# Optimization experiments

Hardware: AMD Instinct MI355X
Metric: run time of the kernel (lower is better)

## Reference

```python
import jax, jax.numpy as jnp
import numpy as np

WS = 4          # window size per axis
HEADS = 3
HEAD_DIM = 32
DIM = 96
DISP = WS // 2  # displacement for shifted windows


def _make_mask(axis):
    # (w^3, w^3) additive mask, -inf across the wrap-around boundary on `axis`
    m = np.zeros((WS, WS, WS, WS, WS, WS), dtype=np.float32)
    d = DISP
    if axis == 0:
        m[-d:, :, :, :-d, :, :] = -np.inf
        m[:-d, :, :, -d:, :, :] = -np.inf
    elif axis == 1:
        m[:, -d:, :, :, :-d, :] = -np.inf
        m[:, :-d, :, :, -d:, :] = -np.inf
    else:
        m[:, :, -d:, :, :, :-d] = -np.inf
        m[:, :, :-d, :, :, -d:] = -np.inf
    return jnp.asarray(m.reshape(WS**3, WS**3))


def setup_inputs() -> dict:
    key = jax.random.key(0)
    k1, k2, k3, k4 = jax.random.split(key, 4)
    inner = HEADS * HEAD_DIM
    x = jax.random.normal(k1, (1, 64, 64, 64, DIM), dtype=jnp.float32)
    w_qkv = jax.random.normal(k2, (3 * inner, DIM), dtype=jnp.float32) * 0.02
    w_out = jax.random.normal(k3, (DIM, inner), dtype=jnp.float32) * 0.02
    b_out = jax.random.normal(k4, (DIM,), dtype=jnp.float32) * 0.02
    return {
        'x': x, 'w_qkv': w_qkv, 'w_out': w_out, 'b_out': b_out,
        'x_mask': _make_mask(0), 'y_mask': _make_mask(1), 'z_mask': _make_mask(2),
    }


def _forward(x, w_qkv, w_out, b_out, x_mask, y_mask, z_mask):
    scale = HEAD_DIM ** -0.5
    b, nx, ny, nz, _ = x.shape
    nwx, nwy, nwz = nx // WS, ny // WS, nz // WS
    seq = WS ** 3
    # cyclic shift by -displacement
    x = jnp.roll(x, shift=(-DISP, -DISP, -DISP), axis=(1, 2, 3))
    qkv = jnp.einsum('bxyzc,oc->bxyzo', x, w_qkv)
    q, k, v = jnp.split(qkv, 3, axis=-1)

    def win(t):  # -> (b, h, n_windows, seq, d)
        t = t.reshape(b, nwx, WS, nwy, WS, nwz, WS, HEADS, HEAD_DIM)
        t = t.transpose(0, 7, 1, 3, 5, 2, 4, 6, 8)
        return t.reshape(b, HEADS, nwx * nwy * nwz, seq, HEAD_DIM)

    q, k, v = win(q), win(k), win(v)
    dots = jnp.einsum('bhwid,bhwjd->bhwij', q, k) * scale

    # shifted-window masking (faithful to original einops relabeling, incl.
    # the final mislabeled rearrange which permutes the window grid)
    d = dots.reshape(b, HEADS, nwx, nwy, nwz, seq, seq)
    d = d.transpose(0, 1, 3, 4, 2, 5, 6)          # (b,h,ny,nz,nx,i,j)
    d = d.at[:, :, :, :, -1].add(x_mask)
    d = d.transpose(0, 1, 4, 3, 2, 5, 6)          # (b,h,nx,nz,ny,i,j)
    d = d.at[:, :, :, :, -1].add(y_mask)
    d = d.transpose(0, 1, 2, 4, 3, 5, 6)          # (b,h,nx,ny,nz,i,j)
    d = d.transpose(0, 1, 4, 2, 3, 5, 6)          # original's final rearrange bug
    dots = d.reshape(b, HEADS, nwx * nwy * nwz, seq, seq)

    attn = jax.nn.softmax(dots, axis=-1)
    out = jnp.einsum('bhwij,bhwjd->bhwid', attn, v)
    # un-window
    out = out.reshape(b, HEADS, nwx, nwy, nwz, WS, WS, WS, HEAD_DIM)
    out = out.transpose(0, 2, 5, 3, 6, 4, 7, 1, 8).reshape(b, nx, ny, nz, HEADS * HEAD_DIM)
    out = jnp.einsum('bxyzc,oc->bxyzo', out, w_out) + b_out
    # cyclic back shift
    return jnp.roll(out, shift=(DISP, DISP, DISP), axis=(1, 2, 3))


def reference(x, w_qkv, w_out, b_out, x_mask, y_mask, z_mask):
    return _forward(x, w_qkv, w_out, b_out, x_mask, y_mask, z_mask)
```

## Files before the change

### kernel.cpp

```cpp
#include <hip/hip_runtime.h>
#include <hip/hip_bf16.h>


using bf4   = __attribute__((ext_vector_type(4))) short;
using bf8   = __attribute__((ext_vector_type(8))) short;
using f32x4 = __attribute__((ext_vector_type(4))) float;

#define SW      100
#define WQ_ROWS 288
#define W_ROWS  384
#define W_SHORTS (W_ROWS * SW)
#define WL_ROWS 192
#define WL_SHORTS (WL_ROWS * SW)

__device__ __forceinline__ short f2b(float f) {
  __hip_bfloat16 h = __float2bfloat16(f);
  return *reinterpret_cast<short*>(&h);
}
__device__ __forceinline__ bf4 pk4(const f32x4& a) {
  bf4 s; s[0] = f2b(a[0]); s[1] = f2b(a[1]); s[2] = f2b(a[2]); s[3] = f2b(a[3]);
  return s;
}
__device__ __forceinline__ bf8 cvt8(const float4& a, const float4& b) {
  bf8 o;
  o[0] = f2b(a.x); o[1] = f2b(a.y); o[2] = f2b(a.z); o[3] = f2b(a.w);
  o[4] = f2b(b.x); o[5] = f2b(b.y); o[6] = f2b(b.z); o[7] = f2b(b.w);
  return o;
}

#if __has_builtin(__builtin_amdgcn_mfma_f32_16x16x16bf16_1k)
__device__ __forceinline__ f32x4 mfma16(bf4 a, bf4 b, f32x4 c) {
  return __builtin_amdgcn_mfma_f32_16x16x16bf16_1k(a, b, c, 0, 0, 0);
}
#elif __has_builtin(__builtin_amdgcn_mfma_f32_16x16x16_bf16)
__device__ __forceinline__ f32x4 mfma16(bf4 a, bf4 b, f32x4 c) {
  return __builtin_amdgcn_mfma_f32_16x16x16_bf16(a, b, c, 0, 0, 0);
}
#else
__device__ __forceinline__ f32x4 mfma16(bf4 a, bf4 b, f32x4 c) {
  asm("v_mfma_f32_16x16x16_bf16 %0, %1, %2, %0" : "+v"(c) : "v"(a), "v"(b));
  return c;
}
#endif

#if __has_builtin(__builtin_amdgcn_exp2f)
__device__ __forceinline__ float exp2n(float x) { return __builtin_amdgcn_exp2f(x); }
#else
__device__ __forceinline__ float exp2n(float x) {
  float r; asm("v_exp_f32 %0, %1" : "=v"(r) : "v"(x)); return r;
}
#endif

__global__ void prep_weights(const float* __restrict__ wq, const float* __restrict__ wo,
                             short* __restrict__ wpk) {
  int i = blockIdx.x * 256 + threadIdx.x;
  if (i >= W_SHORTS) return;
  int row = i / SW, c = i - row * SW;
  const float QS = 0.17677669529663687f * 1.4426950408889634f;
  float v = 0.f;
  if (c < 96) {
    if (row < 96)           v = wq[row * 96 + c] * QS;
    else if (row < WQ_ROWS) v = wq[row * 96 + c];
    else                    v = wo[(row - WQ_ROWS) * 96 + c];
  }
  wpk[i] = f2b(v);
}

__global__ __launch_bounds__(256)
__attribute__((amdgpu_waves_per_eu(1, 2)))
void fused_swin3d(const float* __restrict__ x,
                  const short* __restrict__ wpk,
                  const float* __restrict__ bo,
                  float* __restrict__ out) {
  __shared__ __align__(16) short ls_w[WL_SHORTS];

  const int tid = threadIdx.x;
  const float4* wsrc = reinterpret_cast<const float4*>(wpk);
  #pragma unroll
  for (int i = 0; i < 10; ++i) {
    int c = i * 256 + tid;
    if (c < WL_SHORTS / 8)
      *reinterpret_cast<float4*>(&ls_w[c * 8]) = wsrc[c];
  }

  const int wbase = ((int)blockIdx.x * 4 + (tid >> 6)) * 2;
  const int lane = tid & 63;
  const int lr   = lane & 15;
  const int kg   = lane >> 4;
  const int sy = (lr >> 2) & 3, sz = lr & 3;
  const int ch0 = kg * 8;
  const short* gw_v  = wpk + 192 * SW;
  const short* gw_o  = wpk + WQ_ROWS * SW;

  __syncthreads();

  #pragma unroll
  for (int wi = 0; wi < 2; ++wi) {
    const int w = wbase + wi;
    const int p = w >> 8, q = (w >> 4) & 15, r = w & 15;

    bf4 qn[4][6], kn[4][6], vn[4][6];

    #pragma unroll
    for (int sc = 0; sc < 4; ++sc) {
      const int gx1 = (q * 4 + sc + 2) & 63, gy1 = (r * 4 + sy + 2) & 63, gz1 = (p * 4 + sz + 2) & 63;
      const size_t b1 = (size_t)((gx1 * 64 + gy1) * 64 + gz1) * 96;

      float4 xa0 = *reinterpret_cast<const float4*>(&x[b1 +  0 + ch0]);
      float4 xa1 = *reinterpret_cast<const float4*>(&x[b1 + 32 + ch0]);
      float4 xa2 = *reinterpret_cast<const float4*>(&x[b1 + 64 + ch0]);
      float4 xa3 = *reinterpret_cast<const float4*>(&x[b1 +  0 + ch0 + 4]);
      float4 xa4 = *reinterpret_cast<const float4*>(&x[b1 + 32 + ch0 + 4]);
      float4 xa5 = *reinterpret_cast<const float4*>(&x[b1 + 64 + ch0 + 4]);

      bf8 x1[3];
      x1[0] = cvt8(xa0, xa3); x1[1] = cvt8(xa1, xa4); x1[2] = cvt8(xa2, xa5);

      #pragma unroll
      for (int n = 0; n < 12; ++n) {
        f32x4 acc = {0.f, 0.f, 0.f, 0.f};
        const short* wrow = &ls_w[(n * 16 + lr) * SW + ch0];
        acc = __builtin_amdgcn_mfma_f32_16x16x32_bf16(*reinterpret_cast<const bf8*>(wrow +  0), x1[0], acc, 0, 0, 0);
        acc = __builtin_amdgcn_mfma_f32_16x16x32_bf16(*reinterpret_cast<const bf8*>(wrow + 32), x1[1], acc, 0, 0, 0);
        acc = __builtin_amdgcn_mfma_f32_16x16x32_bf16(*reinterpret_cast<const bf8*>(wrow + 64), x1[2], acc, 0, 0, 0);
        if (n < 6) qn[sc][n] = pk4(acc);
        else       kn[sc][n - 6] = pk4(acc);
      }
    }

    #pragma unroll
    for (int sc = 0; sc < 4; ++sc) {
      const int gx2 = (p * 4 + sc + 2) & 63, gy2 = (q * 4 + sy + 2) & 63, gz2 = (r * 4 + sz + 2) & 63;
      const size_t b2 = (size_t)((gx2 * 64 + gy2) * 64 + gz2) * 96;

      float4 xb0 = *reinterpret_cast<const float4*>(&x[b2 +  0 + ch0]);
      float4 xb1 = *reinterpret_cast<const float4*>(&x[b2 + 32 + ch0]);
      float4 xb2 = *reinterpret_cast<const float4*>(&x[b2 + 64 + ch0]);
      float4 xb3 = *reinterpret_cast<const float4*>(&x[b2 +  0 + ch0 + 4]);
      float4 xb4 = *reinterpret_cast<const float4*>(&x[b2 + 32 + ch0 + 4]);
      float4 xb5 = *reinterpret_cast<const float4*>(&x[b2 + 64 + ch0 + 4]);

      bf8 x2[3];
      x2[0] = cvt8(xb0, xb3); x2[1] = cvt8(xb1, xb4); x2[2] = cvt8(xb2, xb5);

      #pragma unroll
      for (int n = 0; n < 6; ++n) {
        f32x4 acc = {0.f, 0.f, 0.f, 0.f};
        const short* wrow = &gw_v[(n * 16 + lr) * SW + ch0];
        acc = __builtin_amdgcn_mfma_f32_16x16x32_bf16(x2[0], *reinterpret_cast<const bf8*>(wrow +  0), acc, 0, 0, 0);
        acc = __builtin_amdgcn_mfma_f32_16x16x32_bf16(x2[1], *reinterpret_cast<const bf8*>(wrow + 32), acc, 0, 0, 0);
        acc = __builtin_amdgcn_mfma_f32_16x16x32_bf16(x2[2], *reinterpret_cast<const bf8*>(wrow + 64), acc, 0, 0, 0);
        vn[sc][n] = pk4(acc);
      }
    }

    const bool mx = (q == 15), my = (r == 15);
    const bool killy = my && ((lr >= 8) != (kg >= 2));

    #pragma unroll
    for (int qc = 0; qc < 4; ++qc) {
      f32x4 osw[6];
      #pragma unroll
      for (int c = 0; c < 6; ++c) osw[c] = (f32x4){0.f, 0.f, 0.f, 0.f};

      #pragma unroll
      for (int h = 0; h < 3; ++h) {
        f32x4 sv[4];
        __builtin_amdgcn_s_setprio(1);
        #pragma unroll
        for (int nj = 0; nj < 4; ++nj) {
          f32x4 z = {0.f, 0.f, 0.f, 0.f};
          z = mfma16(kn[nj][2 * h + 0], qn[qc][2 * h + 0], z);
          sv[nj] = mfma16(kn[nj][2 * h + 1], qn[qc][2 * h + 1], z);
        }
        __builtin_amdgcn_s_setprio(0);
        float ps[4];
        #pragma unroll
        for (int nj = 0; nj < 4; ++nj) {
          const bool kill = killy || (mx && ((qc >= 2) != (nj >= 2)));
          #pragma unroll
          for (int t = 0; t < 4; ++t)
            sv[nj][t] = kill ? 0.f : exp2n(sv[nj][t]);
          ps[nj] = (sv[nj][0] + sv[nj][1]) + (sv[nj][2] + sv[nj][3]);
        }
        float sum = (ps[0] + ps[1]) + (ps[2] + ps[3]);
        bf4 pb[4];
        #pragma unroll
        for (int t = 0; t < 4; ++t) pb[t] = pk4(sv[t]);
        sum += __shfl_xor(sum, 16);
        sum += __shfl_xor(sum, 32);
        __builtin_amdgcn_s_setprio(1);
        #pragma unroll
        for (int nc = 0; nc < 2; ++nc)
          #pragma unroll
          for (int t = 0; t < 4; ++t)
            osw[2 * h + nc] = mfma16(vn[t][2 * h + nc], pb[t], osw[2 * h + nc]);
        __builtin_amdgcn_s_setprio(0);
        const float inv = 1.f / sum;
        #pragma unroll
        for (int nc = 0; nc < 2; ++nc)
          #pragma unroll
          for (int t = 0; t < 4; ++t)
            osw[2 * h + nc][t] *= inv;
      }

      bf4 ofr[6];
      #pragma unroll
      for (int c = 0; c < 6; ++c) ofr[c] = pk4(osw[c]);

      const int gx2 = (p * 4 + qc + 2) & 63, gy2 = (q * 4 + sy + 2) & 63, gz2 = (r * 4 + sz + 2) & 63;
      const size_t b2 = (size_t)((gx2 * 64 + gy2) * 64 + gz2) * 96;
      #pragma unroll
      for (int no = 0; no < 6; ++no) {
        f32x4 acc = {0.f, 0.f, 0.f, 0.f};
        const short* wr = &gw_o[(no * 16 + lr) * SW + kg * 4];
        #pragma unroll
        for (int c = 0; c < 6; ++c) {
          bf4 wa = *reinterpret_cast<const bf4*>(wr + c * 16);
          acc = mfma16(wa, ofr[c], acc);
        }
        const float4 bb = *reinterpret_cast<const float4*>(&bo[no * 16 + kg * 4]);
        float4 o4;
        o4.x = acc[0] + bb.x; o4.y = acc[1] + bb.y;
        o4.z = acc[2] + bb.z; o4.w = acc[3] + bb.w;
        *reinterpret_cast<float4*>(&out[b2 + no * 16 + kg * 4]) = o4;
      }
    }
  }
}

extern "C" void kernel_launch(void* const* d_in, const int* in_sizes, int n_in,
                              void* d_out, int out_size, void* d_ws, size_t ws_size,
                              hipStream_t stream) {
  const float* x  = (const float*)d_in[0];
  const float* wq = (const float*)d_in[1];
  const float* wo = (const float*)d_in[2];
  const float* bo = (const float*)d_in[3];

  short* wpk = (short*)d_ws;

  prep_weights<<<(W_SHORTS + 255) / 256, 256, 0, stream>>>(wq, wo, wpk);
  fused_swin3d<<<512, 256, 0, stream>>>(x, wpk, bo, (float*)d_out);
}
```

Measured before the change: 106.6 us.

## Process one window per wave and pre-pack output weights per lane

Each wave now handles a single window instead of two, and the grid doubles to 1024 blocks, which raises parallelism and shortens each wave's serial work. The prep kernel additionally writes a lane-ordered copy of the output projection weights, so the out-projection loads three 16-byte vectors per lane instead of six 8-byte strided loads. In exchange, each block still copies the shared QK weights into LDS, but now amortises that copy over half as many windows, and the extra prep pass adds a little work.

After: 94.52 us. 1.13x faster.

```diff
diff --git a/kernel.cpp b/kernel.cpp
--- a/kernel.cpp
+++ b/kernel.cpp
@@ -12,6 +12,7 @@
 #define W_SHORTS (W_ROWS * SW)
 #define WL_ROWS 192
 #define WL_SHORTS (WL_ROWS * SW)
+#define OPK_SHORTS (6 * 64 * 24)
 
 __device__ __forceinline__ short f2b(float f) {
   __hip_bfloat16 h = __float2bfloat16(f);
@@ -54,16 +55,24 @@
 __global__ void prep_weights(const float* __restrict__ wq, const float* __restrict__ wo,
                              short* __restrict__ wpk) {
   int i = blockIdx.x * 256 + threadIdx.x;
-  if (i >= W_SHORTS) return;
-  int row = i / SW, c = i - row * SW;
   const float QS = 0.17677669529663687f * 1.4426950408889634f;
-  float v = 0.f;
-  if (c < 96) {
-    if (row < 96)           v = wq[row * 96 + c] * QS;
-    else if (row < WQ_ROWS) v = wq[row * 96 + c];
-    else                    v = wo[(row - WQ_ROWS) * 96 + c];
-  }
-  wpk[i] = f2b(v);
+  if (i < W_SHORTS) {
+    int row = i / SW, c = i - row * SW;
+    float v = 0.f;
+    if (c < 96) {
+      if (row < 96)           v = wq[row * 96 + c] * QS;
+      else if (row < WQ_ROWS) v = wq[row * 96 + c];
+      else                    v = wo[(row - WQ_ROWS) * 96 + c];
+    }
+    wpk[i] = f2b(v);
+  } else if (i < W_SHORTS + OPK_SHORTS) {
+    int j = i - W_SHORTS;
+    int rec = j / 24, ce = j - rec * 24;
+    int c = ce >> 2, e = ce & 3;
+    int no = rec >> 6, lane = rec & 63;
+    int kg = lane >> 4, lr = lane & 15;
+    wpk[i] = f2b(wo[(no * 16 + lr) * 96 + c * 16 + kg * 4 + e]);
+  }
 }
 
 __global__ __launch_bounds__(256)
@@ -83,148 +92,147 @@
       *reinterpret_cast<float4*>(&ls_w[c * 8]) = wsrc[c];
   }
 
-  const int wbase = ((int)blockIdx.x * 4 + (tid >> 6)) * 2;
+  const int w = (int)blockIdx.x * 4 + (tid >> 6);
+  const int p = w >> 8, q = (w >> 4) & 15, r = w & 15;
   const int lane = tid & 63;
   const int lr   = lane & 15;
   const int kg   = lane >> 4;
   const int sy = (lr >> 2) & 3, sz = lr & 3;
   const int ch0 = kg * 8;
-  const short* gw_v  = wpk + 192 * SW;
-  const short* gw_o  = wpk + WQ_ROWS * SW;
+  const short* gw_v = wpk + 192 * SW;
+  const short* opk  = wpk + W_SHORTS;
 
   __syncthreads();
 
-  #pragma unroll
-  for (int wi = 0; wi < 2; ++wi) {
-    const int w = wbase + wi;
-    const int p = w >> 8, q = (w >> 4) & 15, r = w & 15;
-
-    bf4 qn[4][6], kn[4][6], vn[4][6];
-
-    #pragma unroll
-    for (int sc = 0; sc < 4; ++sc) {
-      const int gx1 = (q * 4 + sc + 2) & 63, gy1 = (r * 4 + sy + 2) & 63, gz1 = (p * 4 + sz + 2) & 63;
-      const size_t b1 = (size_t)((gx1 * 64 + gy1) * 64 + gz1) * 96;
-
-      float4 xa0 = *reinterpret_cast<const float4*>(&x[b1 +  0 + ch0]);
-      float4 xa1 = *reinterpret_cast<const float4*>(&x[b1 + 32 + ch0]);
-      float4 xa2 = *reinterpret_cast<const float4*>(&x[b1 + 64 + ch0]);
-      float4 xa3 = *reinterpret_cast<const float4*>(&x[b1 +  0 + ch0 + 4]);
-      float4 xa4 = *reinterpret_cast<const float4*>(&x[b1 + 32 + ch0 + 4]);
-      float4 xa5 = *reinterpret_cast<const float4*>(&x[b1 + 64 + ch0 + 4]);
-
-      bf8 x1[3];
-      x1[0] = cvt8(xa0, xa3); x1[1] = cvt8(xa1, xa4); x1[2] = cvt8(xa2, xa5);
-
-      #pragma unroll
-      for (int n = 0; n < 12; ++n) {
-        f32x4 acc = {0.f, 0.f, 0.f, 0.f};
-        const short* wrow = &ls_w[(n * 16 + lr) * SW + ch0];
-        acc = __builtin_amdgcn_mfma_f32_16x16x32_bf16(*reinterpret_cast<const bf8*>(wrow +  0), x1[0], acc, 0, 0, 0);
-        acc = __builtin_amdgcn_mfma_f32_16x16x32_bf16(*reinterpret_cast<const bf8*>(wrow + 32), x1[1], acc, 0, 0, 0);
-        acc = __builtin_amdgcn_mfma_f32_16x16x32_bf16(*reinterpret_cast<const bf8*>(wrow + 64), x1[2], acc, 0, 0, 0);
-        if (n < 6) qn[sc][n] = pk4(acc);
-        else       kn[sc][n - 6] = pk4(acc);
+  bf4 qn[4][6], kn[4][6], vn[4][6];
+
+  #pragma unroll
+  for (int sc = 0; sc < 4; ++sc) {
+    const int gx1 = (q * 4 + sc + 2) & 63, gy1 = (r * 4 + sy + 2) & 63, gz1 = (p * 4 + sz + 2) & 63;
+    const size_t b1 = (size_t)((gx1 * 64 + gy1) * 64 + gz1) * 96;
+
+    float4 xa0 = *reinterpret_cast<const float4*>(&x[b1 +  0 + ch0]);
+    float4 xa1 = *reinterpret_cast<const float4*>(&x[b1 + 32 + ch0]);
+    float4 xa2 = *reinterpret_cast<const float4*>(&x[b1 + 64 + ch0]);
+    float4 xa3 = *reinterpret_cast<const float4*>(&x[b1 +  0 + ch0 + 4]);
+    float4 xa4 = *reinterpret_cast<const float4*>(&x[b1 + 32 + ch0 + 4]);
+    float4 xa5 = *reinterpret_cast<const float4*>(&x[b1 + 64 + ch0 + 4]);
+
+    bf8 x1[3];
+    x1[0] = cvt8(xa0, xa3); x1[1] = cvt8(xa1, xa4); x1[2] = cvt8(xa2, xa5);
+
+    #pragma unroll
+    for (int n = 0; n < 12; ++n) {
+      f32x4 acc = {0.f, 0.f, 0.f, 0.f};
+      const short* wrow = &ls_w[(n * 16 + lr) * SW + ch0];
+      acc = __builtin_amdgcn_mfma_f32_16x16x32_bf16(*reinterpret_cast<const bf8*>(wrow +  0), x1[0], acc, 0, 0, 0);
+      acc = __builtin_amdgcn_mfma_f32_16x16x32_bf16(*reinterpret_cast<const bf8*>(wrow + 32), x1[1], acc, 0, 0, 0);
+      acc = __builtin_amdgcn_mfma_f32_16x16x32_bf16(*reinterpret_cast<const bf8*>(wrow + 64), x1[2], acc, 0, 0, 0);
+      if (n < 6) qn[sc][n] = pk4(acc);
+      else       kn[sc][n - 6] = pk4(acc);
+    }
+  }
+
+  #pragma unroll
+  for (int sc = 0; sc < 4; ++sc) {
+    const int gx2 = (p * 4 + sc + 2) & 63, gy2 = (q * 4 + sy + 2) & 63, gz2 = (r * 4 + sz + 2) & 63;
+    const size_t b2 = (size_t)((gx2 * 64 + gy2) * 64 + gz2) * 96;
+
+    float4 xb0 = *reinterpret_cast<const float4*>(&x[b2 +  0 + ch0]);
+    float4 xb1 = *reinterpret_cast<const float4*>(&x[b2 + 32 + ch0]);
+    float4 xb2 = *reinterpret_cast<const float4*>(&x[b2 + 64 + ch0]);
+    float4 xb3 = *reinterpret_cast<const float4*>(&x[b2 +  0 + ch0 + 4]);
+    float4 xb4 = *reinterpret_cast<const float4*>(&x[b2 + 32 + ch0 + 4]);
+    float4 xb5 = *reinterpret_cast<const float4*>(&x[b2 + 64 + ch0 + 4]);
+
+    bf8 x2[3];
+    x2[0] = cvt8(xb0, xb3); x2[1] = cvt8(xb1, xb4); x2[2] = cvt8(xb2, xb5);
+
+    #pragma unroll
+    for (int n = 0; n < 6; ++n) {
+      f32x4 acc = {0.f, 0.f, 0.f, 0.f};
+      const short* wrow = &gw_v[(n * 16 + lr) * SW + ch0];
+      acc = __builtin_amdgcn_mfma_f32_16x16x32_bf16(x2[0], *reinterpret_cast<const bf8*>(wrow +  0), acc, 0, 0, 0);
+      acc = __builtin_amdgcn_mfma_f32_16x16x32_bf16(x2[1], *reinterpret_cast<const bf8*>(wrow + 32), acc, 0, 0, 0);
+      acc = __builtin_amdgcn_mfma_f32_16x16x32_bf16(x2[2], *reinterpret_cast<const bf8*>(wrow + 64), acc, 0, 0, 0);
+      vn[sc][n] = pk4(acc);
+    }
+  }
+
+  const bool mx = (q == 15), my = (r == 15);
+  const bool killy = my && ((lr >= 8) != (kg >= 2));
+
+  #pragma unroll
+  for (int qc = 0; qc < 4; ++qc) {
+    f32x4 osw[6];
+    #pragma unroll
+    for (int c = 0; c < 6; ++c) osw[c] = (f32x4){0.f, 0.f, 0.f, 0.f};
+
+    #pragma unroll
+    for (int h = 0; h < 3; ++h) {
+      f32x4 sv[4];
+      __builtin_amdgcn_s_setprio(1);
+      #pragma unroll
+      for (int nj = 0; nj < 4; ++nj) {
+        f32x4 z = {0.f, 0.f, 0.f, 0.f};
+        z = mfma16(kn[nj][2 * h + 0], qn[qc][2 * h + 0], z);
+        sv[nj] = mfma16(kn[nj][2 * h + 1], qn[qc][2 * h + 1], z);
       }
-    }
-
-    #pragma unroll
-    for (int sc = 0; sc < 4; ++sc) {
-      const int gx2 = (p * 4 + sc + 2) & 63, gy2 = (q * 4 + sy + 2) & 63, gz2 = (r * 4 + sz + 2) & 63;
-      const size_t b2 = (size_t)((gx2 * 64 + gy2) * 64 + gz2) * 96;
-
-      float4 xb0 = *reinterpret_cast<const float4*>(&x[b2 +  0 + ch0]);
-      float4 xb1 = *reinterpret_cast<const float4*>(&x[b2 + 32 + ch0]);
-      float4 xb2 = *reinterpret_cast<const float4*>(&x[b2 + 64 + ch0]);
-      float4 xb3 = *reinterpret_cast<const float4*>(&x[b2 +  0 + ch0 + 4]);
-      float4 xb4 = *reinterpret_cast<const float4*>(&x[b2 + 32 + ch0 + 4]);
-      float4 xb5 = *reinterpret_cast<const float4*>(&x[b2 + 64 + ch0 + 4]);
-
-      bf8 x2[3];
-      x2[0] = cvt8(xb0, xb3); x2[1] = cvt8(xb1, xb4); x2[2] = cvt8(xb2, xb5);
-
-      #pragma unroll
-      for (int n = 0; n < 6; ++n) {
-        f32x4 acc = {0.f, 0.f, 0.f, 0.f};
-        const short* wrow = &gw_v[(n * 16 + lr) * SW + ch0];
-        acc = __builtin_amdgcn_mfma_f32_16x16x32_bf16(x2[0], *reinterpret_cast<const bf8*>(wrow +  0), acc, 0, 0, 0);
-        acc = __builtin_amdgcn_mfma_f32_16x16x32_bf16(x2[1], *reinterpret_cast<const bf8*>(wrow + 32), acc, 0, 0, 0);
-        acc = __builtin_amdgcn_mfma_f32_16x16x32_bf16(x2[2], *reinterpret_cast<const bf8*>(wrow + 64), acc, 0, 0, 0);
-        vn[sc][n] = pk4(acc);
+      __builtin_amdgcn_s_setprio(0);
+      float ps[4];
+      #pragma unroll
+      for (int nj = 0; nj < 4; ++nj) {
+        const bool kill = killy || (mx && ((qc >= 2) != (nj >= 2)));
+        #pragma unroll
+        for (int t = 0; t < 4; ++t)
+          sv[nj][t] = kill ? 0.f : exp2n(sv[nj][t]);
+        ps[nj] = (sv[nj][0] + sv[nj][1]) + (sv[nj][2] + sv[nj][3]);
       }
-    }
-
-    const bool mx = (q == 15), my = (r == 15);
-    const bool killy = my && ((lr >= 8) != (kg >= 2));
-
-    #pragma unroll
-    for (int qc = 0; qc < 4; ++qc) {
-      f32x4 osw[6];
-      #pragma unroll
-      for (int c = 0; c < 6; ++c) osw[c] = (f32x4){0.f, 0.f, 0.f, 0.f};
-
-      #pragma unroll
-      for (int h = 0; h < 3; ++h) {
-        f32x4 sv[4];
-        __builtin_amdgcn_s_setprio(1);
+      float sum = (ps[0] + ps[1]) + (ps[2] + ps[3]);
+      bf4 pb[4];
+      #pragma unroll
+      for (int t = 0; t < 4; ++t) pb[t] = pk4(sv[t]);
+      sum += __shfl_xor(sum, 16);
+      sum += __shfl_xor(sum, 32);
+      __builtin_amdgcn_s_setprio(1);
+      #pragma unroll
+      for (int nc = 0; nc < 2; ++nc)
         #pragma unroll
-        for (int nj = 0; nj < 4; ++nj) {
-          f32x4 z = {0.f, 0.f, 0.f, 0.f};
-          z = mfma16(kn[nj][2 * h + 0], qn[qc][2 * h + 0], z);
-          sv[nj] = mfma16(kn[nj][2 * h + 1], qn[qc][2 * h + 1], z);
-        }
-        __builtin_amdgcn_s_setprio(0);
-        float ps[4];
+        for (int t = 0; t < 4; ++t)
+          osw[2 * h + nc] = mfma16(vn[t][2 * h + nc], pb[t], osw[2 * h + nc]);
+      __builtin_amdgcn_s_setprio(0);
+      const float inv = 1.f / sum;
+      #pragma unroll
+      for (int nc = 0; nc < 2; ++nc)
         #pragma unroll
-        for (int nj = 0; nj < 4; ++nj) {
-          const bool kill = killy || (mx && ((qc >= 2) != (nj >= 2)));
-          #pragma unroll
-          for (int t = 0; t < 4; ++t)
-            sv[nj][t] = kill ? 0.f : exp2n(sv[nj][t]);
-          ps[nj] = (sv[nj][0] + sv[nj][1]) + (sv[nj][2] + sv[nj][3]);
-        }
-        float sum = (ps[0] + ps[1]) + (ps[2] + ps[3]);
-        bf4 pb[4];
-        #pragma unroll
-        for (int t = 0; t < 4; ++t) pb[t] = pk4(sv[t]);
-        sum += __shfl_xor(sum, 16);
-        sum += __shfl_xor(sum, 32);
-        __builtin_amdgcn_s_setprio(1);
-        #pragma unroll
-        for (int nc = 0; nc < 2; ++nc)
-          #pragma unroll
-          for (int t = 0; t < 4; ++t)
-            osw[2 * h + nc] = mfma16(vn[t][2 * h + nc], pb[t], osw[2 * h + nc]);
-        __builtin_amdgcn_s_setprio(0);
-        const float inv = 1.f / sum;
-        #pragma unroll
-        for (int nc = 0; nc < 2; ++nc)
-          #pragma unroll
-          for (int t = 0; t < 4; ++t)
-            osw[2 * h + nc][t] *= inv;
-      }
-
-      bf4 ofr[6];
-      #pragma unroll
-      for (int c = 0; c < 6; ++c) ofr[c] = pk4(osw[c]);
-
-      const int gx2 = (p * 4 + qc + 2) & 63, gy2 = (q * 4 + sy + 2) & 63, gz2 = (r * 4 + sz + 2) & 63;
-      const size_t b2 = (size_t)((gx2 * 64 + gy2) * 64 + gz2) * 96;
-      #pragma unroll
-      for (int no = 0; no < 6; ++no) {
-        f32x4 acc = {0.f, 0.f, 0.f, 0.f};
-        const short* wr = &gw_o[(no * 16 + lr) * SW + kg * 4];
-        #pragma unroll
-        for (int c = 0; c < 6; ++c) {
-          bf4 wa = *reinterpret_cast<const bf4*>(wr + c * 16);
-          acc = mfma16(wa, ofr[c], acc);
-        }
-        const float4 bb = *reinterpret_cast<const float4*>(&bo[no * 16 + kg * 4]);
-        float4 o4;
-        o4.x = acc[0] + bb.x; o4.y = acc[1] + bb.y;
-        o4.z = acc[2] + bb.z; o4.w = acc[3] + bb.w;
-        *reinterpret_cast<float4*>(&out[b2 + no * 16 + kg * 4]) = o4;
-      }
+        for (int t = 0; t < 4; ++t)
+          osw[2 * h + nc][t] *= inv;
+    }
+
+    bf4 ofr[6];
+    #pragma unroll
+    for (int c = 0; c < 6; ++c) ofr[c] = pk4(osw[c]);
+
+    const int gx2 = (p * 4 + qc + 2) & 63, gy2 = (q * 4 + sy + 2) & 63, gz2 = (r * 4 + sz + 2) & 63;
+    const size_t b2 = (size_t)((gx2 * 64 + gy2) * 64 + gz2) * 96;
+    #pragma unroll
+    for (int no = 0; no < 6; ++no) {
+      const short* wr = &opk[(no * 64 + lane) * 24];
+      bf8 w01 = *reinterpret_cast<const bf8*>(wr);
+      bf8 w23 = *reinterpret_cast<const bf8*>(wr + 8);
+      bf8 w45 = *reinterpret_cast<const bf8*>(wr + 16);
+      f32x4 acc = {0.f, 0.f, 0.f, 0.f};
+      acc = mfma16(__builtin_shufflevector(w01, w01, 0, 1, 2, 3), ofr[0], acc);
+      acc = mfma16(__builtin_shufflevector(w01, w01, 4, 5, 6, 7), ofr[1], acc);
+      acc = mfma16(__builtin_shufflevector(w23, w23, 0, 1, 2, 3), ofr[2], acc);
+      acc = mfma16(__builtin_shufflevector(w23, w23, 4, 5, 6, 7), ofr[3], acc);
+      acc = mfma16(__builtin_shufflevector(w45, w45, 0, 1, 2, 3), ofr[4], acc);
+      acc = mfma16(__builtin_shufflevector(w45, w45, 4, 5, 6, 7), ofr[5], acc);
+      const float4 bb = *reinterpret_cast<const float4*>(&bo[no * 16 + kg * 4]);
+      float4 o4;
+      o4.x = acc[0] + bb.x; o4.y = acc[1] + bb.y;
+      o4.z = acc[2] + bb.z; o4.w = acc[3] + bb.w;
+      *reinterpret_cast<float4*>(&out[b2 + no * 16 + kg * 4]) = o4;
     }
   }
 }
@@ -239,6 +247,6 @@
 
   short* wpk = (short*)d_ws;
 
-  prep_weights<<<(W_SHORTS + 255) / 256, 256, 0, stream>>>(wq, wo, wpk);
-  fused_swin3d<<<512, 256, 0, stream>>>(x, wpk, bo, (float*)d_out);
-}
+  prep_weights<<<(W_SHORTS + OPK_SHORTS + 255) / 256, 256, 0, stream>>>(wq, wo, wpk);
+  fused_swin3d<<<1024, 256, 0, stream>>>(x, wpk, bo, (float*)d_out);
+}
```
